# Optimization experiments

Measured on AMD Instinct MI355X. Metric: run time of the kernel, lower is better.

## Reference

```python
import jax, jax.numpy as jnp
import numpy as np


def setup_inputs() -> dict:
    key = jax.random.key(0)
    k1, k2, k3 = jax.random.split(key, 3)
    B, L, H = 8, 2048, 256
    g = jax.random.normal(k1, (B, L, H), dtype=jnp.float32)
    # nn.Linear weights: stored as [out_features, in_features]
    WP = jax.random.normal(k2, (H, H), dtype=jnp.float32) * (1.0 / np.sqrt(H))
    W_out = jax.random.normal(k3, (H, 3 * H), dtype=jnp.float32) * (1.0 / np.sqrt(3 * H))
    b_out = jnp.zeros((H,), dtype=jnp.float32)
    return {"g": g, "WP": WP, "W_out": W_out, "b_out": b_out}


def reference(g, WP, W_out, b_out):
    # Wh = WP(g): [B, L, H] @ WP^T
    Wh = jnp.einsum("blh,oh->blo", g, WP)
    # s_t = bmm(Wh, g^T): [B, L, L]  (rows indexed by Wh positions, cols by g positions)
    s_t = jnp.einsum("bih,bjh->bij", Wh, g)
    # softmax over dim=1 (the first L axis, non-standard)
    a_t = jax.nn.softmax(s_t, axis=1)
    # c_t = bmm(a_t, g): [B, L, H]
    c_t = jnp.einsum("bij,bjh->bih", a_t, g)
    out = jnp.concatenate((g, c_t, g * c_t), axis=2)  # [B, L, 3H]
    out = jnp.einsum("blk,ok->blo", out, W_out) + b_out
    return jax.nn.relu(out)
```

## Files before the change

kernel.cpp:

```cpp
#include <hip/hip_runtime.h>
#include <math.h>

static constexpr int  Bb = 8;
static constexpr int  L  = 2048;
static constexpr int  H  = 256;
static constexpr long BL = (long)Bb * L;
static constexpr long LH = (long)L * H;
static constexpr long LL = (long)L * L;
static constexpr int  NCH = 16;

typedef __attribute__((ext_vector_type(8))) unsigned short u16x8;
typedef __attribute__((ext_vector_type(4))) unsigned short u16x4;
typedef __attribute__((ext_vector_type(8))) _Float16       f16x8;
typedef __attribute__((ext_vector_type(4))) float          f32x4;

__device__ __forceinline__ unsigned short f2hu(float x) {
    union { _Float16 h; unsigned short u; } v; v.h = (_Float16)x; return v.u;
}
__device__ __forceinline__ float hu2f(unsigned short u) {
    union { unsigned short u; _Float16 h; } v; v.u = u; return (float)v.h;
}
__device__ __forceinline__ void gl_lds16(const unsigned short* g, unsigned short* l) {
    __builtin_amdgcn_global_load_lds(
        (const __attribute__((address_space(1))) unsigned int*)g,
        (__attribute__((address_space(3))) unsigned int*)l, 16, 0, 0);
}

__global__ __launch_bounds__(256)
void cvt_g(const float* __restrict__ x, unsigned short* __restrict__ h)
{
    const long i = ((long)blockIdx.x * 256 + threadIdx.x) * 4;
    float4 v = *(const float4*)(x + i);
    u16x4 o;
    o[0] = f2hu(v.x); o[1] = f2hu(v.y); o[2] = f2hu(v.z); o[3] = f2hu(v.w);
    *(u16x4*)(h + i) = o;
}

__global__ __launch_bounds__(256)
void cvt_two(const float* __restrict__ x1, unsigned short* __restrict__ h1,
             const float* __restrict__ x2, unsigned short* __restrict__ h2)
{
    const float* x; unsigned short* hp; long base;
    if (blockIdx.x < 64) { x = x1; hp = h1; base = (long)blockIdx.x * 1024; }
    else { x = x2; hp = h2; base = (long)(blockIdx.x - 64) * 1024; }
    const long i = base + (long)threadIdx.x * 4;
    float4 v = *(const float4*)(x + i);
    u16x4 o;
    o[0] = f2hu(v.x); o[1] = f2hu(v.y); o[2] = f2hu(v.z); o[3] = f2hu(v.w);
    *(u16x4*)(hp + i) = o;
}

__global__ __launch_bounds__(256)
void transpose_h16(const unsigned short* __restrict__ in, unsigned short* __restrict__ out)
{
    __shared__ unsigned short T[32][33];
    const int b = blockIdx.z, j0 = blockIdx.x * 32, h0 = blockIdx.y * 32;
    const int t = threadIdx.x, r = t >> 3, c4 = (t & 7) << 2;
    const unsigned short* inb = in + (long)b * LH;
    unsigned short* outb = out + (long)b * LH;
    u16x4 v = *(const u16x4*)(inb + (long)(j0 + r) * H + h0 + c4);
#pragma unroll
    for (int e = 0; e < 4; ++e) T[r][c4 + e] = v[e];
    __syncthreads();
    u16x4 w;
#pragma unroll
    for (int e = 0; e < 4; ++e) w[e] = T[c4 + e][r];
    *(u16x4*)(outb + (long)(h0 + r) * L + j0 + c4) = w;
}

__global__ __launch_bounds__(256)
void col_stats_r(const float* __restrict__ pm, const float* __restrict__ pz,
                 float* __restrict__ rfac)
{
    const long idx = (long)blockIdx.x * 256 + threadIdx.x;
    const long b = idx / L, j = idx - b * L;
    const float* pmb = pm + b * (long)NCH * L + j;
    const float* pzb = pz + b * (long)NCH * L + j;
    float m = -1e30f;
#pragma unroll
    for (int c = 0; c < NCH; ++c) m = fmaxf(m, pmb[(long)c * L]);
    float z = 0.f;
#pragma unroll
    for (int c = 0; c < NCH; ++c) z += pzb[(long)c * L] * __expf(pmb[(long)c * L] - m);
    const float zi = 1.f / z;
    float* rb = rfac + b * (long)NCH * L + j;
#pragma unroll
    for (int c = 0; c < NCH; ++c) rb[(long)c * L] = __expf(pmb[(long)c * L] - m) * zi;
}

template<int MODE, int NSEG>
__global__ __launch_bounds__(256)
void mfma_nt(const unsigned short* A0, const unsigned short* A1, const unsigned short* A2,
             const unsigned short* B0, const unsigned short* B1, const unsigned short* B2,
             float* __restrict__ C, unsigned short* __restrict__ Ch,
             float* __restrict__ pm, float* __restrict__ pz,
             const float* __restrict__ bias,
             int N, int lda, int ldb,
             long strideA, long strideB, long strideC)
{
    __shared__ __align__(16) unsigned short As[128][32];
    __shared__ __align__(16) unsigned short Bs[128][32];
    __shared__ float smx[2][128];
    __shared__ float szx[2][128];
    __shared__ float colm[128];
    const int tid  = threadIdx.x;
    const int wid  = tid >> 6, lane = tid & 63;
    const int wm   = wid >> 1, wn = wid & 1;
    const long b   = blockIdx.z;
    const int m0   = blockIdx.x * 128, n0 = blockIdx.y * 128;
    const int lrow = tid >> 2, lkc = (tid & 3) << 3;
    const int frow = lane & 15, fk = (lane >> 4) << 3;
    f32x4 acc[4][4];
#pragma unroll
    for (int i = 0; i < 4; ++i)
#pragma unroll
        for (int j = 0; j < 4; ++j) acc[i][j] = (f32x4){0.f, 0.f, 0.f, 0.f};

    const long abase = b * strideA, bbase = b * strideB;
    unsigned short* AsW = &As[0][0] + ((tid >> 6) << 9);
    unsigned short* BsW = &Bs[0][0] + ((tid >> 6) << 9);

    for (int seg = 0; seg < NSEG; ++seg) {
        const unsigned short* Ap = (seg == 0) ? A0 : ((seg == 1) ? A1 : A2);
        const unsigned short* Bp = (seg == 0) ? B0 : ((seg == 1) ? B1 : B2);
        for (int k0 = 0; k0 < 256; k0 += 32) {
            if (MODE == 1) {
                __syncthreads();
#pragma unroll
                for (int r = 0; r < 2; ++r) {
                    const int row = lrow + (r << 6);
                    u16x8 av;
                    if (seg == 2) {
                        const long off = (long)(m0 + row) * lda + k0 + lkc;
                        u16x8 gv = *(const u16x8*)(A0 + off);
                        u16x8 cv = *(const u16x8*)(A1 + off);
#pragma unroll
                        for (int e = 0; e < 8; ++e)
                            av[e] = f2hu(hu2f(gv[e]) * hu2f(cv[e]));
                    } else {
                        av = *(const u16x8*)(Ap + (long)(m0 + row) * lda + k0 + lkc);
                    }
                    *(u16x8*)&As[row][lkc] = av;
                    u16x8 bv = *(const u16x8*)(Bp + (long)(n0 + row) * ldb + k0 + lkc);
                    *(u16x8*)&Bs[row][lkc] = bv;
                }
                __syncthreads();
            } else {
                const unsigned short* Abase = Ap + abase + (long)m0 * lda + k0;
                const unsigned short* Bbase = Bp + bbase + (long)n0 * ldb + k0;
                __syncthreads();
#pragma unroll
                for (int r = 0; r < 2; ++r) {
                    gl_lds16(Abase + (long)(lrow + (r << 6)) * lda + lkc, AsW + (r << 11));
                    gl_lds16(Bbase + (long)(lrow + (r << 6)) * ldb + lkc, BsW + (r << 11));
                }
                __syncthreads();
            }
            f16x8 af[4], bfv[4];
#pragma unroll
            for (int i = 0; i < 4; ++i) af[i]  = *(const f16x8*)&As[wm * 64 + i * 16 + frow][fk];
#pragma unroll
            for (int j = 0; j < 4; ++j) bfv[j] = *(const f16x8*)&Bs[wn * 64 + j * 16 + frow][fk];
#pragma unroll
            for (int i = 0; i < 4; ++i)
#pragma unroll
                for (int j = 0; j < 4; ++j)
                    acc[i][j] = __builtin_amdgcn_mfma_f32_16x16x32_f16(af[i], bfv[j], acc[i][j], 0, 0, 0);
        }
    }

    if (MODE == 0) {
#pragma unroll
        for (int j = 0; j < 4; ++j) {
            float m = -1e30f;
#pragma unroll
            for (int i = 0; i < 4; ++i)
#pragma unroll
                for (int e = 0; e < 4; ++e) m = fmaxf(m, acc[i][j][e]);
            m = fmaxf(m, __shfl_xor(m, 16));
            m = fmaxf(m, __shfl_xor(m, 32));
            if ((lane >> 4) == 0) smx[wm][wn * 64 + j * 16 + frow] = m;
        }
        __syncthreads();
        if (tid < 128) colm[tid] = fmaxf(smx[0][tid], smx[1][tid]);
        __syncthreads();
        unsigned short* Pb = Ch + b * strideC;
#pragma unroll
        for (int j = 0; j < 4; ++j) {
            const int colL = wn * 64 + j * 16 + frow;
            const float mm = colm[colL];
            float z = 0.f;
#pragma unroll
            for (int i = 0; i < 4; ++i) {
                const int rbase = m0 + wm * 64 + i * 16 + ((lane >> 4) << 2);
#pragma unroll
                for (int e = 0; e < 4; ++e) {
                    float p = __expf(acc[i][j][e] - mm);
                    z += p;
                    Pb[(long)(rbase + e) * N + (n0 + colL)] = f2hu(p);
                }
            }
            z += __shfl_xor(z, 16);
            z += __shfl_xor(z, 32);
            if ((lane >> 4) == 0) szx[wm][colL] = z;
        }
        __syncthreads();
        if (tid < 128) {
            const long o = ((long)b * NCH + blockIdx.x) * L + n0 + tid;
            pm[o] = colm[tid];
            pz[o] = szx[0][tid] + szx[1][tid];
        }
    } else {
#pragma unroll
        for (int i = 0; i < 4; ++i)
#pragma unroll
            for (int j = 0; j < 4; ++j) {
                const int rbase = m0 + wm * 64 + i * 16 + ((lane >> 4) << 2);
                const int col   = n0 + wn * 64 + j * 16 + frow;
                if (MODE == 2) {
#pragma unroll
                    for (int e = 0; e < 4; ++e)
                        Ch[(long)(rbase + e) * N + col] = f2hu(acc[i][j][e]);
                } else {
                    float* Cb = C + b * strideC;
                    const float bv = bias[col];
#pragma unroll
                    for (int e = 0; e < 4; ++e)
                        Cb[(long)(rbase + e) * N + col] = fmaxf(acc[i][j][e] + bv, 0.f);
                }
            }
    }
}

__global__ __launch_bounds__(256)
void attn_av(const unsigned short* __restrict__ P, const float* __restrict__ rfac,
             const unsigned short* __restrict__ gT, unsigned short* __restrict__ ch)
{
    __shared__ __align__(16) unsigned short As[32][32];
    __shared__ __align__(16) unsigned short Bs[256][32];
    const int t = threadIdx.x, b = blockIdx.z;
    const int i0 = blockIdx.x * 32;
    const int chunk = i0 >> 7;
    const int w = t >> 6, l = t & 63;
    const int frow = l & 15, fk = (l >> 4) << 3;
    const unsigned short* Pb  = P + (long)b * LL;
    const float* rrow = rfac + ((long)b * NCH + chunk) * L;
    const unsigned short* gTb = gT + (long)b * LH;
    unsigned short* cb = ch + (long)b * LH;

    const int ar = t >> 3, ac = (t & 7) << 2;
    const int brow = t >> 2, bc = (t & 3) << 3;
    unsigned short* BsW = &Bs[0][0] + ((t >> 6) << 9);

    f32x4 acc[2][4];
#pragma unroll
    for (int i = 0; i < 2; ++i)
#pragma unroll
        for (int j = 0; j < 4; ++j) acc[i][j] = (f32x4){0.f, 0.f, 0.f, 0.f};

    const unsigned short* Prow = Pb + (long)(i0 + ar) * L + ac;

    for (int j0 = 0; j0 < L; j0 += 32) {
        __syncthreads();
        u16x4 p4 = *(const u16x4*)(Prow + j0);
        float4 r4 = *(const float4*)(rrow + j0 + ac);
        u16x4 a;
        a[0] = f2hu(hu2f(p4[0]) * r4.x);
        a[1] = f2hu(hu2f(p4[1]) * r4.y);
        a[2] = f2hu(hu2f(p4[2]) * r4.z);
        a[3] = f2hu(hu2f(p4[3]) * r4.w);
        *(u16x4*)&As[ar][ac] = a;
#pragma unroll
        for (int r = 0; r < 4; ++r)
            gl_lds16(gTb + (long)((r << 6) + brow) * L + j0 + bc, BsW + (r << 11));
        __syncthreads();
        f16x8 af[2], bfv[4];
#pragma unroll
        for (int i = 0; i < 2; ++i) af[i]  = *(const f16x8*)&As[i * 16 + frow][fk];
#pragma unroll
        for (int j = 0; j < 4; ++j) bfv[j] = *(const f16x8*)&Bs[w * 64 + j * 16 + frow][fk];
#pragma unroll
        for (int i = 0; i < 2; ++i)
#pragma unroll
            for (int j = 0; j < 4; ++j)
                acc[i][j] = __builtin_amdgcn_mfma_f32_16x16x32_f16(af[i], bfv[j], acc[i][j], 0, 0, 0);
    }
#pragma unroll
    for (int i = 0; i < 2; ++i)
#pragma unroll
        for (int j = 0; j < 4; ++j) {
            const int rbase = i0 + i * 16 + ((l >> 4) << 2);
            const int col   = w * 64 + j * 16 + frow;
#pragma unroll
            for (int e = 0; e < 4; ++e)
                cb[(long)(rbase + e) * H + col] = f2hu(acc[i][j][e]);
        }
}

extern "C" void kernel_launch(void* const* d_in, const int* in_sizes, int n_in,
                              void* d_out, int out_size, void* d_ws, size_t ws_size,
                              hipStream_t stream)
{
    const float* g     = (const float*)d_in[0];
    const float* WP    = (const float*)d_in[1];
    const float* W_out = (const float*)d_in[2];
    const float* b_out = (const float*)d_in[3];
    float* out = (float*)d_out;

    char* w = (char*)d_ws;
    unsigned short* P    = (unsigned short*)w;
    unsigned short* gh   = (unsigned short*)(w + 67108864);
    unsigned short* ch   = (unsigned short*)(w + 75497472);
    unsigned short* gT   = (unsigned short*)(w + 83886080);
    unsigned short* Whh  = (unsigned short*)(w + 92274688);
    unsigned short* WPh  = (unsigned short*)(w + 100663296);
    unsigned short* Woh  = (unsigned short*)(w + 100794368);
    float*          pm   = (float*)(w + 101187584);
    float*          pz   = (float*)(w + 102236160);
    float*          rfac = (float*)(w + 103284736);

    cvt_g<<<dim3((int)(BL * H / 1024)), 256, 0, stream>>>(g, gh);
    cvt_two<<<dim3(256), 256, 0, stream>>>(WP, WPh, W_out, Woh);

    mfma_nt<2, 1><<<dim3((int)(BL / 128), H / 128, 1), 256, 0, stream>>>(
        gh, nullptr, nullptr, WPh, nullptr, nullptr, nullptr, Whh,
        nullptr, nullptr, nullptr, H, H, H, 0, 0, 0);

    mfma_nt<0, 1><<<dim3(L / 128, L / 128, Bb), 256, 0, stream>>>(
        Whh, nullptr, nullptr, gh, nullptr, nullptr, nullptr, P,
        pm, pz, nullptr, L, H, H, LH, LH, LL);

    col_stats_r<<<dim3((int)(BL / 256)), 256, 0, stream>>>(pm, pz, rfac);

    transpose_h16<<<dim3(L / 32, H / 32, Bb), 256, 0, stream>>>(gh, gT);

    attn_av<<<dim3(L / 32, 1, Bb), 256, 0, stream>>>(P, rfac, gT, ch);

    mfma_nt<1, 3><<<dim3((int)(BL / 128), H / 128, 1), 256, 0, stream>>>(
        gh, ch, nullptr, Woh, Woh + 256, Woh + 512, out, nullptr,
        nullptr, nullptr, b_out, H, H, 3 * H, 0, 0, 0);
}
```

Before: 197.9 us.

## Stage P tile in LDS for coalesced stores; pipeline attn_av with 4-stage LDS ring

The score kernel now writes the exponentiated P tile into a padded shared-memory buffer and then stores it to global memory as 16-byte coalesced rows, replacing scattered 2-byte stores. attn_av is restructured into a 4-buffer, 64 KB dynamic-LDS pipeline. It issues async global-to-LDS loads of gT two steps ahead with an XOR swizzle against bank conflicts, loads P and the row factors directly into registers, and applies the scaling in f16 vector math. Hand-placed waitcnt and barrier instructions replace the two syncthreads per iteration. The cost is more LDS per block, which lowers occupancy, plus some precision loss from doing the scale multiply in f16.

After: 218.7 us. 1.11x slower.

```diff
diff --git a/kernel.cpp b/kernel.cpp
--- a/kernel.cpp
+++ b/kernel.cpp
@@ -103,6 +103,7 @@
     __shared__ float smx[2][128];
     __shared__ float szx[2][128];
     __shared__ float colm[128];
+    __shared__ __align__(16) unsigned short Ps[(MODE == 0) ? 128 : 1][136];
     const int tid  = threadIdx.x;
     const int wid  = tid >> 6, lane = tid & 63;
     const int wm   = wid >> 1, wn = wid & 1;
@@ -184,7 +185,6 @@
         __syncthreads();
         if (tid < 128) colm[tid] = fmaxf(smx[0][tid], smx[1][tid]);
         __syncthreads();
-        unsigned short* Pb = Ch + b * strideC;
 #pragma unroll
         for (int j = 0; j < 4; ++j) {
             const int colL = wn * 64 + j * 16 + frow;
@@ -192,12 +192,12 @@
             float z = 0.f;
 #pragma unroll
             for (int i = 0; i < 4; ++i) {
-                const int rbase = m0 + wm * 64 + i * 16 + ((lane >> 4) << 2);
+                const int rl = wm * 64 + i * 16 + ((lane >> 4) << 2);
 #pragma unroll
                 for (int e = 0; e < 4; ++e) {
                     float p = __expf(acc[i][j][e] - mm);
                     z += p;
-                    Pb[(long)(rbase + e) * N + (n0 + colL)] = f2hu(p);
+                    Ps[rl + e][colL] = f2hu(p);
                 }
             }
             z += __shfl_xor(z, 16);
@@ -205,6 +205,14 @@
             if ((lane >> 4) == 0) szx[wm][colL] = z;
         }
         __syncthreads();
+        unsigned short* Pb = Ch + b * strideC;
+        const int q = lane >> 4, c16 = lane & 15;
+#pragma unroll
+        for (int e2 = 0; e2 < 8; ++e2) {
+            const int rl = e2 * 16 + wid * 4 + q;
+            u16x8 v = *(const u16x8*)&Ps[rl][c16 * 8];
+            *(u16x8*)(Pb + (long)(m0 + rl) * N + n0 + c16 * 8) = v;
+        }
         if (tid < 128) {
             const long o = ((long)b * NCH + blockIdx.x) * L + n0 + tid;
             pm[o] = colm[tid];
@@ -236,8 +244,7 @@
 void attn_av(const unsigned short* __restrict__ P, const float* __restrict__ rfac,
              const unsigned short* __restrict__ gT, unsigned short* __restrict__ ch)
 {
-    __shared__ __align__(16) unsigned short As[32][32];
-    __shared__ __align__(16) unsigned short Bs[256][32];
+    extern __shared__ unsigned short BsD[];
     const int t = threadIdx.x, b = blockIdx.z;
     const int i0 = blockIdx.x * 32;
     const int chunk = i0 >> 7;
@@ -248,9 +255,25 @@
     const unsigned short* gTb = gT + (long)b * LH;
     unsigned short* cb = ch + (long)b * LH;
 
-    const int ar = t >> 3, ac = (t & 7) << 2;
-    const int brow = t >> 2, bc = (t & 3) << 3;
-    unsigned short* BsW = &Bs[0][0] + ((t >> 6) << 9);
+    const unsigned short* bsrc[4];
+#pragma unroll
+    for (int r = 0; r < 4; ++r) {
+        const int rp  = r * 32 + (t >> 3);
+        const int q16 = (t & 7) << 3;
+        const int ua  = q16 ^ ((rp & 7) << 3);
+        const int hh  = rp * 2 + (ua >> 5);
+        bsrc[r] = gTb + (long)hh * L + (ua & 31);
+    }
+    int boff[4];
+#pragma unroll
+    for (int j4 = 0; j4 < 4; ++j4) {
+        const int hrow = w * 64 + j4 * 16 + frow;
+        const int rp = hrow >> 1;
+        const int u  = ((hrow & 1) << 5) + fk;
+        boff[j4] = rp * 64 + (u ^ ((rp & 7) << 3));
+    }
+    const unsigned short* prow0 = Pb + (long)(i0 + frow) * L + fk;
+    const unsigned short* prow1 = Pb + (long)(i0 + 16 + frow) * L + fk;
 
     f32x4 acc[2][4];
 #pragma unroll
@@ -258,33 +281,70 @@
 #pragma unroll
         for (int j = 0; j < 4; ++j) acc[i][j] = (f32x4){0.f, 0.f, 0.f, 0.f};
 
-    const unsigned short* Prow = Pb + (long)(i0 + ar) * L + ac;
-
-    for (int j0 = 0; j0 < L; j0 += 32) {
-        __syncthreads();
-        u16x4 p4 = *(const u16x4*)(Prow + j0);
-        float4 r4 = *(const float4*)(rrow + j0 + ac);
-        u16x4 a;
-        a[0] = f2hu(hu2f(p4[0]) * r4.x);
-        a[1] = f2hu(hu2f(p4[1]) * r4.y);
-        a[2] = f2hu(hu2f(p4[2]) * r4.z);
-        a[3] = f2hu(hu2f(p4[3]) * r4.w);
-        *(u16x4*)&As[ar][ac] = a;
-#pragma unroll
-        for (int r = 0; r < 4; ++r)
-            gl_lds16(gTb + (long)((r << 6) + brow) * L + j0 + bc, BsW + (r << 11));
-        __syncthreads();
-        f16x8 af[2], bfv[4];
-#pragma unroll
-        for (int i = 0; i < 2; ++i) af[i]  = *(const f16x8*)&As[i * 16 + frow][fk];
-#pragma unroll
-        for (int j = 0; j < 4; ++j) bfv[j] = *(const f16x8*)&Bs[w * 64 + j * 16 + frow][fk];
-#pragma unroll
-        for (int i = 0; i < 2; ++i)
-#pragma unroll
-            for (int j = 0; j < 4; ++j)
-                acc[i][j] = __builtin_amdgcn_mfma_f32_16x16x32_f16(af[i], bfv[j], acc[i][j], 0, 0, 0);
-    }
+    u16x8 pA0, pA1, pB0, pB1;
+    float4 rAa, rAb, rBa, rBb;
+
+#define STAGE_B(BUF, J)                                                     \
+    {                                                                       \
+        unsigned short* dst = BsD + (BUF) * 8192 + w * 512;                 \
+        _Pragma("unroll")                                                   \
+        for (int r = 0; r < 4; ++r)                                         \
+            gl_lds16(bsrc[r] + (J), dst + r * 2048);                        \
+    }
+
+    STAGE_B(0, 0)
+    STAGE_B(1, 32)
+    __builtin_amdgcn_sched_barrier(0);
+    pA0 = *(const u16x8*)(prow0);          pA1 = *(const u16x8*)(prow1);
+    rAa = *(const float4*)(rrow + fk);     rAb = *(const float4*)(rrow + fk + 4);
+    pB0 = *(const u16x8*)(prow0 + 32);     pB1 = *(const u16x8*)(prow1 + 32);
+    rBa = *(const float4*)(rrow + 32 + fk); rBb = *(const float4*)(rrow + 32 + fk + 4);
+    __builtin_amdgcn_sched_barrier(0);
+    asm volatile("s_waitcnt vmcnt(8)" ::: "memory");
+    __builtin_amdgcn_sched_barrier(0);
+    __builtin_amdgcn_s_barrier();
+
+#define STEP(PH, C, P0V, P1V, RAV, RBV)                                     \
+    {                                                                       \
+        const int jS = ((C) + 2) * 32;                                      \
+        if (jS < L) STAGE_B(((PH) + 2) & 3, jS)                             \
+        __builtin_amdgcn_sched_barrier(0);                                  \
+        f16x8 rh;                                                           \
+        rh[0] = (_Float16)RAV.x; rh[1] = (_Float16)RAV.y;                   \
+        rh[2] = (_Float16)RAV.z; rh[3] = (_Float16)RAV.w;                   \
+        rh[4] = (_Float16)RBV.x; rh[5] = (_Float16)RBV.y;                   \
+        rh[6] = (_Float16)RBV.z; rh[7] = (_Float16)RBV.w;                   \
+        f16x8 a0 = *(f16x8*)&P0V * rh;                                      \
+        f16x8 a1 = *(f16x8*)&P1V * rh;                                      \
+        _Pragma("unroll")                                                   \
+        for (int j4 = 0; j4 < 4; ++j4) {                                    \
+            f16x8 bf = *(const f16x8*)(BsD + (PH) * 8192 + boff[j4]);       \
+            acc[0][j4] = __builtin_amdgcn_mfma_f32_16x16x32_f16(a0, bf, acc[0][j4], 0, 0, 0); \
+            acc[1][j4] = __builtin_amdgcn_mfma_f32_16x16x32_f16(a1, bf, acc[1][j4], 0, 0, 0); \
+        }                                                                   \
+        if (jS < L) {                                                       \
+            P0V = *(const u16x8*)(prow0 + jS);                              \
+            P1V = *(const u16x8*)(prow1 + jS);                              \
+            RAV = *(const float4*)(rrow + jS + fk);                         \
+            RBV = *(const float4*)(rrow + jS + fk + 4);                     \
+        }                                                                   \
+        __builtin_amdgcn_sched_barrier(0);                                  \
+        if ((C) >= 61) { asm volatile("s_waitcnt vmcnt(0)" ::: "memory"); } \
+        else           { asm volatile("s_waitcnt vmcnt(8)" ::: "memory"); } \
+        __builtin_amdgcn_sched_barrier(0);                                  \
+        __builtin_amdgcn_s_barrier();                                       \
+    }
+
+    for (int cc = 0; cc < 16; ++cc) {
+        const int c0 = cc * 4;
+        STEP(0, c0 + 0, pA0, pA1, rAa, rAb)
+        STEP(1, c0 + 1, pB0, pB1, rBa, rBb)
+        STEP(2, c0 + 2, pA0, pA1, rAa, rAb)
+        STEP(3, c0 + 3, pB0, pB1, rBa, rBb)
+    }
+#undef STEP
+#undef STAGE_B
+
 #pragma unroll
     for (int i = 0; i < 2; ++i)
 #pragma unroll
@@ -334,7 +394,7 @@
 
     transpose_h16<<<dim3(L / 32, H / 32, Bb), 256, 0, stream>>>(gh, gT);
 
-    attn_av<<<dim3(L / 32, 1, Bb), 256, 0, stream>>>(P, rfac, gT, ch);
+    attn_av<<<dim3(L / 32, 1, Bb), 256, 65536, stream>>>(P, rfac, gT, ch);
 
     mfma_nt<1, 3><<<dim3((int)(BL / 128), H / 128, 1), 256, 0, stream>>>(
         gh, ch, nullptr, Woh, Woh + 256, Woh + 512, out, nullptr,
```

## Store P and gT in MFMA fragment-tiled layouts so attn_av loads directly without LDS

Applied to the files above, without the earlier changes.

The score GEMM now computes the transposed product (g·Wh^T), so softmax reductions run along rows within a block. P is written in a 16x16 fragment-tiled layout with vectorized u16x4 stores instead of scattered 2-byte stores. The transpose kernel emits gT in a fragment-packed layout too, which lets attn_av read A and B operands straight from global memory into registers. That removes its LDS staging and __syncthreads. Normalization factors are stored as fp16 and applied with a packed half multiply, which costs some precision and relies on caches for operand reuse.

New measurement: 201.6 us. No clear change (+1.9%).

```diff
diff --git a/kernel.cpp b/kernel.cpp
--- a/kernel.cpp
+++ b/kernel.cpp
@@ -51,26 +51,30 @@
 }
 
 __global__ __launch_bounds__(256)
-void transpose_h16(const unsigned short* __restrict__ in, unsigned short* __restrict__ out)
+void transpose_h16(const unsigned short* __restrict__ in, unsigned short* __restrict__ outf)
 {
     __shared__ unsigned short T[32][33];
     const int b = blockIdx.z, j0 = blockIdx.x * 32, h0 = blockIdx.y * 32;
     const int t = threadIdx.x, r = t >> 3, c4 = (t & 7) << 2;
     const unsigned short* inb = in + (long)b * LH;
-    unsigned short* outb = out + (long)b * LH;
+    unsigned short* ob = outf + (long)b * LH;
     u16x4 v = *(const u16x4*)(inb + (long)(j0 + r) * H + h0 + c4);
 #pragma unroll
     for (int e = 0; e < 4; ++e) T[r][c4 + e] = v[e];
     __syncthreads();
-    u16x4 w;
-#pragma unroll
-    for (int e = 0; e < 4; ++e) w[e] = T[c4 + e][r];
-    *(u16x4*)(outb + (long)(h0 + r) * L + j0 + c4) = w;
+    const int f = t >> 7, lam = (t & 127) >> 1, half = t & 1;
+    const int hloc  = f * 16 + (lam & 15);
+    const int jbase = half * 16 + (lam >> 4) * 4;
+    u16x4 o;
+#pragma unroll
+    for (int d = 0; d < 4; ++d) o[d] = T[jbase + d][hloc];
+    *(u16x4*)(ob + ((long)((h0 >> 4) + f) * (L / 32) + (j0 >> 5)) * 512
+                 + lam * 8 + half * 4) = o;
 }
 
 __global__ __launch_bounds__(256)
 void col_stats_r(const float* __restrict__ pm, const float* __restrict__ pz,
-                 float* __restrict__ rfac)
+                 unsigned short* __restrict__ r16)
 {
     const long idx = (long)blockIdx.x * 256 + threadIdx.x;
     const long b = idx / L, j = idx - b * L;
@@ -83,9 +87,9 @@
 #pragma unroll
     for (int c = 0; c < NCH; ++c) z += pzb[(long)c * L] * __expf(pmb[(long)c * L] - m);
     const float zi = 1.f / z;
-    float* rb = rfac + b * (long)NCH * L + j;
-#pragma unroll
-    for (int c = 0; c < NCH; ++c) rb[(long)c * L] = __expf(pmb[(long)c * L] - m) * zi;
+    unsigned short* rb = r16 + b * (long)NCH * L + j;
+#pragma unroll
+    for (int c = 0; c < NCH; ++c) rb[(long)c * L] = f2hu(__expf(pmb[(long)c * L] - m) * zi);
 }
 
 template<int MODE, int NSEG>
@@ -170,43 +174,61 @@
     }
 
     if (MODE == 0) {
-#pragma unroll
-        for (int j = 0; j < 4; ++j) {
-            float m = -1e30f;
-#pragma unroll
-            for (int i = 0; i < 4; ++i)
-#pragma unroll
-                for (int e = 0; e < 4; ++e) m = fmaxf(m, acc[i][j][e]);
-            m = fmaxf(m, __shfl_xor(m, 16));
-            m = fmaxf(m, __shfl_xor(m, 32));
-            if ((lane >> 4) == 0) smx[wm][wn * 64 + j * 16 + frow] = m;
+        const int q = lane >> 4, c16 = lane & 15;
+        float rm[4][4];
+#pragma unroll
+        for (int ja = 0; ja < 4; ++ja)
+#pragma unroll
+            for (int e = 0; e < 4; ++e) {
+                float m = fmaxf(fmaxf(acc[ja][0][e], acc[ja][1][e]),
+                                fmaxf(acc[ja][2][e], acc[ja][3][e]));
+                m = fmaxf(m, __shfl_xor(m, 1));
+                m = fmaxf(m, __shfl_xor(m, 2));
+                m = fmaxf(m, __shfl_xor(m, 4));
+                m = fmaxf(m, __shfl_xor(m, 8));
+                rm[ja][e] = m;
+            }
+        if (c16 == 0) {
+#pragma unroll
+            for (int ja = 0; ja < 4; ++ja)
+#pragma unroll
+                for (int e = 0; e < 4; ++e)
+                    smx[wn][wm * 64 + ja * 16 + q * 4 + e] = rm[ja][e];
         }
         __syncthreads();
         if (tid < 128) colm[tid] = fmaxf(smx[0][tid], smx[1][tid]);
         __syncthreads();
-        unsigned short* Pb = Ch + b * strideC;
-#pragma unroll
-        for (int j = 0; j < 4; ++j) {
-            const int colL = wn * 64 + j * 16 + frow;
-            const float mm = colm[colL];
-            float z = 0.f;
-#pragma unroll
-            for (int i = 0; i < 4; ++i) {
-                const int rbase = m0 + wm * 64 + i * 16 + ((lane >> 4) << 2);
+        unsigned short* Pt = Ch + b * strideC;
+#pragma unroll
+        for (int ja = 0; ja < 4; ++ja) {
+            float mm[4];
+#pragma unroll
+            for (int e = 0; e < 4; ++e) mm[e] = colm[wm * 64 + ja * 16 + q * 4 + e];
+            float zr[4] = {0.f, 0.f, 0.f, 0.f};
+#pragma unroll
+            for (int ib = 0; ib < 4; ++ib) {
+                u16x4 pv;
 #pragma unroll
                 for (int e = 0; e < 4; ++e) {
-                    float p = __expf(acc[i][j][e] - mm);
-                    z += p;
-                    Pb[(long)(rbase + e) * N + (n0 + colL)] = f2hu(p);
+                    float p = __expf(acc[ja][ib][e] - mm[e]);
+                    zr[e] += p;
+                    pv[e] = f2hu(p);
                 }
-            }
-            z += __shfl_xor(z, 16);
-            z += __shfl_xor(z, 32);
-            if ((lane >> 4) == 0) szx[wm][colL] = z;
+                const long ti = (n0 >> 4) + wn * 4 + ib;
+                const long tj = (m0 >> 4) + wm * 4 + ja;
+                *(u16x4*)(Pt + (ti * (L / 16) + tj) * 256 + lane * 4) = pv;
+            }
+#pragma unroll
+            for (int e = 0; e < 4; ++e) {
+                float z = zr[e];
+                z += __shfl_xor(z, 1); z += __shfl_xor(z, 2);
+                z += __shfl_xor(z, 4); z += __shfl_xor(z, 8);
+                if (c16 == 0) szx[wn][wm * 64 + ja * 16 + q * 4 + e] = z;
+            }
         }
         __syncthreads();
         if (tid < 128) {
-            const long o = ((long)b * NCH + blockIdx.x) * L + n0 + tid;
+            const long o = ((long)b * NCH + blockIdx.y) * L + m0 + tid;
             pm[o] = colm[tid];
             pz[o] = szx[0][tid] + szx[1][tid];
         }
@@ -233,64 +255,50 @@
 }
 
 __global__ __launch_bounds__(256)
-void attn_av(const unsigned short* __restrict__ P, const float* __restrict__ rfac,
-             const unsigned short* __restrict__ gT, unsigned short* __restrict__ ch)
-{
-    __shared__ __align__(16) unsigned short As[32][32];
-    __shared__ __align__(16) unsigned short Bs[256][32];
+void attn_av(const unsigned short* __restrict__ P, const unsigned short* __restrict__ r16,
+             const unsigned short* __restrict__ gTf, unsigned short* __restrict__ ch)
+{
     const int t = threadIdx.x, b = blockIdx.z;
     const int i0 = blockIdx.x * 32;
-    const int chunk = i0 >> 7;
-    const int w = t >> 6, l = t & 63;
-    const int frow = l & 15, fk = (l >> 4) << 3;
-    const unsigned short* Pb  = P + (long)b * LL;
-    const float* rrow = rfac + ((long)b * NCH + chunk) * L;
-    const unsigned short* gTb = gT + (long)b * LH;
+    const int w = t >> 6, l = t & 63, q = l >> 4, c16 = l & 15;
+    const unsigned short* Pb0 = P + (long)b * LL + ((long)(i0 >> 4) * 128) * 256 + l * 4;
+    const unsigned short* Pb1 = Pb0 + 128 * 256;
+    const unsigned short* rb  = r16 + ((long)b * NCH + (i0 >> 7)) * L;
+    const unsigned short* Bb0 = gTf + (long)b * LH + ((long)(w * 4) * 64) * 512 + l * 8;
     unsigned short* cb = ch + (long)b * LH;
 
-    const int ar = t >> 3, ac = (t & 7) << 2;
-    const int brow = t >> 2, bc = (t & 3) << 3;
-    unsigned short* BsW = &Bs[0][0] + ((t >> 6) << 9);
-
     f32x4 acc[2][4];
 #pragma unroll
     for (int i = 0; i < 2; ++i)
 #pragma unroll
         for (int j = 0; j < 4; ++j) acc[i][j] = (f32x4){0.f, 0.f, 0.f, 0.f};
 
-    const unsigned short* Prow = Pb + (long)(i0 + ar) * L + ac;
-
-    for (int j0 = 0; j0 < L; j0 += 32) {
-        __syncthreads();
-        u16x4 p4 = *(const u16x4*)(Prow + j0);
-        float4 r4 = *(const float4*)(rrow + j0 + ac);
-        u16x4 a;
-        a[0] = f2hu(hu2f(p4[0]) * r4.x);
-        a[1] = f2hu(hu2f(p4[1]) * r4.y);
-        a[2] = f2hu(hu2f(p4[2]) * r4.z);
-        a[3] = f2hu(hu2f(p4[3]) * r4.w);
-        *(u16x4*)&As[ar][ac] = a;
-#pragma unroll
-        for (int r = 0; r < 4; ++r)
-            gl_lds16(gTb + (long)((r << 6) + brow) * L + j0 + bc, BsW + (r << 11));
-        __syncthreads();
-        f16x8 af[2], bfv[4];
-#pragma unroll
-        for (int i = 0; i < 2; ++i) af[i]  = *(const f16x8*)&As[i * 16 + frow][fk];
-#pragma unroll
-        for (int j = 0; j < 4; ++j) bfv[j] = *(const f16x8*)&Bs[w * 64 + j * 16 + frow][fk];
-#pragma unroll
-        for (int i = 0; i < 2; ++i)
-#pragma unroll
-            for (int j = 0; j < 4; ++j)
-                acc[i][j] = __builtin_amdgcn_mfma_f32_16x16x32_f16(af[i], bfv[j], acc[i][j], 0, 0, 0);
+#pragma unroll 2
+    for (int s = 0; s < 64; ++s) {
+        union { u16x4 u[2]; f16x8 h; } a0v, a1v, rv;
+        a0v.u[0] = *(const u16x4*)(Pb0 + (2 * s    ) * 256);
+        a0v.u[1] = *(const u16x4*)(Pb0 + (2 * s + 1) * 256);
+        a1v.u[0] = *(const u16x4*)(Pb1 + (2 * s    ) * 256);
+        a1v.u[1] = *(const u16x4*)(Pb1 + (2 * s + 1) * 256);
+        rv.u[0]  = *(const u16x4*)(rb + s * 32 + q * 4);
+        rv.u[1]  = *(const u16x4*)(rb + s * 32 + 16 + q * 4);
+        f16x8 a0 = a0v.h * rv.h;
+        f16x8 a1 = a1v.h * rv.h;
+#pragma unroll
+        for (int j4 = 0; j4 < 4; ++j4) {
+            u16x8 bu = *(const u16x8*)(Bb0 + ((long)j4 * 64 + s) * 512);
+            f16x8 bf = *(f16x8*)&bu;
+            acc[0][j4] = __builtin_amdgcn_mfma_f32_16x16x32_f16(a0, bf, acc[0][j4], 0, 0, 0);
+            acc[1][j4] = __builtin_amdgcn_mfma_f32_16x16x32_f16(a1, bf, acc[1][j4], 0, 0, 0);
+        }
     }
+
 #pragma unroll
     for (int i = 0; i < 2; ++i)
 #pragma unroll
         for (int j = 0; j < 4; ++j) {
-            const int rbase = i0 + i * 16 + ((l >> 4) << 2);
-            const int col   = w * 64 + j * 16 + frow;
+            const int rbase = i0 + i * 16 + q * 4;
+            const int col   = w * 64 + j * 16 + c16;
 #pragma unroll
             for (int e = 0; e < 4; ++e)
                 cb[(long)(rbase + e) * H + col] = f2hu(acc[i][j][e]);
@@ -311,13 +319,13 @@
     unsigned short* P    = (unsigned short*)w;
     unsigned short* gh   = (unsigned short*)(w + 67108864);
     unsigned short* ch   = (unsigned short*)(w + 75497472);
-    unsigned short* gT   = (unsigned short*)(w + 83886080);
+    unsigned short* gTf  = (unsigned short*)(w + 83886080);
     unsigned short* Whh  = (unsigned short*)(w + 92274688);
     unsigned short* WPh  = (unsigned short*)(w + 100663296);
     unsigned short* Woh  = (unsigned short*)(w + 100794368);
     float*          pm   = (float*)(w + 101187584);
     float*          pz   = (float*)(w + 102236160);
-    float*          rfac = (float*)(w + 103284736);
+    unsigned short* r16  = (unsigned short*)(w + 103284736);
 
     cvt_g<<<dim3((int)(BL * H / 1024)), 256, 0, stream>>>(g, gh);
     cvt_two<<<dim3(256), 256, 0, stream>>>(WP, WPh, W_out, Woh);
@@ -327,14 +335,14 @@
         nullptr, nullptr, nullptr, H, H, H, 0, 0, 0);
 
     mfma_nt<0, 1><<<dim3(L / 128, L / 128, Bb), 256, 0, stream>>>(
-        Whh, nullptr, nullptr, gh, nullptr, nullptr, nullptr, P,
+        gh, nullptr, nullptr, Whh, nullptr, nullptr, nullptr, P,
         pm, pz, nullptr, L, H, H, LH, LH, LL);
 
-    col_stats_r<<<dim3((int)(BL / 256)), 256, 0, stream>>>(pm, pz, rfac);
-
-    transpose_h16<<<dim3(L / 32, H / 32, Bb), 256, 0, stream>>>(gh, gT);
-
-    attn_av<<<dim3(L / 32, 1, Bb), 256, 0, stream>>>(P, rfac, gT, ch);
+    col_stats_r<<<dim3((int)(BL / 256)), 256, 0, stream>>>(pm, pz, r16);
+
+    transpose_h16<<<dim3(L / 32, H / 32, Bb), 256, 0, stream>>>(gh, gTf);
+
+    attn_av<<<dim3(L / 32, 1, Bb), 256, 0, stream>>>(P, r16, gTf, ch);
 
     mfma_nt<1, 3><<<dim3((int)(BL / 128), H / 128, 1), 256, 0, stream>>>(
         gh, ch, nullptr, Woh, Woh + 256, Woh + 512, out, nullptr,
```
